# Performance work log

Measured on AMD Instinct MI355X. Metric: run time of the kernel, lower is better.

The kernel has to match this reference:

```python
import jax, jax.numpy as jnp
import numpy as np

L, BAT, A, B, D, NBITS = 2, 32, 64, 1024, 128, 1024
PADDING = 0


def setup_inputs() -> dict:
    key = jax.random.key(0)
    k1, k2, k3, k4, k5 = jax.random.split(key, 5)
    query_embed = jax.random.normal(k1, (L, BAT, A, D), dtype=jnp.float32)
    doc_embed = jax.random.normal(k2, (L, BAT, B, D), dtype=jnp.float32)
    query_tok = jax.random.randint(k3, (BAT, A), 0, 2)
    doc_tok = jax.random.randint(k4, (BAT, B), 0, 2)
    # LSH projection matrix: randn * sigma + mu with sigma=0.1, mu=0
    r = jax.random.normal(k5, (NBITS, D), dtype=jnp.float32) * 0.1
    return {"query_embed": query_embed, "doc_embed": doc_embed,
            "query_tok": query_tok, "doc_tok": doc_tok, "r": r}


def reference(query_embed, doc_embed, query_tok, doc_tok, r):
    d = r.shape[0]  # num_bits
    # sign-hash: (emb @ r.T > 0).float()  -> binary codes in {0,1}
    c1 = (jnp.einsum('lbad,kd->lbak', query_embed, r) > 0).astype(jnp.float32)  # [L,BAT,A,NBITS]
    c2 = (jnp.einsum('lbcd,kd->lbck', doc_embed, r) > 0).astype(jnp.float32)    # [L,BAT,B,NBITS]
    # Hamming distance via popcount identity: |u-v|_H = sum(u) + sum(v) - 2 u.v
    s1 = c1.sum(-1)  # [L,BAT,A]
    s2 = c2.sum(-1)  # [L,BAT,B]
    dot = jnp.einsum('lbak,lbck->lbac', c1, c2)  # [L,BAT,A,B]
    ham = s1[..., :, None] + s2[..., None, :] - 2.0 * dot
    sim = jnp.cos(jnp.pi / d * ham)  # [L,BAT,A,B]
    # zero out padded query / doc positions
    qmask = (query_tok == PADDING)[None, :, :, None]
    dmask = (doc_tok == PADDING)[None, :, None, :]
    sim = jnp.where(qmask | dmask, 0.0, sim)
    # torch.stack(simmat, dim=1) -> [BAT, L, A, B]
    return jnp.transpose(sim, (1, 0, 2, 3))
```

## Files before the change

### kernel.cpp

```cpp
#include <hip/hip_runtime.h>
#include <math.h>

#define L_ 2
#define BAT_ 32
#define A_ 64
#define B_ 1024
#define D_ 128
#define NBITS_ 1024
#define NW 32
#define NQROWS (L_*BAT_*A_)
#define NDROWS (L_*BAT_*B_)
#define NROWS (NQROWS + NDROWS)

#define TM 128
#define TN 128
#define KH 64
#define RS 136

typedef __bf16 bf16x4 __attribute__((ext_vector_type(4)));
typedef __bf16 bf16x8 __attribute__((ext_vector_type(8)));
typedef float  f32x4  __attribute__((ext_vector_type(4)));

__global__ __launch_bounds__(256) void hash_kernel(
    const float* __restrict__ qe, const float* __restrict__ de,
    const float* __restrict__ r, unsigned int* __restrict__ codes)
{
    __shared__ __align__(16) __bf16 As[TM * RS];
    __shared__ __align__(16) __bf16 Bs[TN * RS];

    const int t = threadIdx.x;
    const int row0 = blockIdx.x * TM;
    const int bit0 = blockIdx.y * TN;

    const float* abase = (row0 < NQROWS) ? (qe + (size_t)row0 * D_)
                                         : (de + (size_t)(row0 - NQROWS) * D_);
    const float* bbase = r + (size_t)bit0 * D_;

    const int wv   = t >> 6;
    const int lane = t & 63;
    const int quad = lane >> 4;
    const int col  = lane & 15;
    const int wrow = (wv >> 1) * 64;
    const int wbit = (wv & 1) * 64;

    f32x4 acc[4][4];
    #pragma unroll
    for (int ti = 0; ti < 4; ++ti)
        #pragma unroll
        for (int tj = 0; tj < 4; ++tj)
            acc[ti][tj] = (f32x4){0.f, 0.f, 0.f, 0.f};

    #pragma unroll
    for (int ks = 0; ks < D_; ks += KH) {
        if (ks) __syncthreads();
        #pragma unroll
        for (int i = 0; i < 8; ++i) {
            int f = (t + i * 256) * 4;
            int rr = f >> 6, cc = f & 63;
            float4 v = *(const float4*)(abase + (size_t)rr * D_ + ks + cc);
            bf16x4 hi, lo;
            hi[0] = (__bf16)v.x; hi[1] = (__bf16)v.y;
            hi[2] = (__bf16)v.z; hi[3] = (__bf16)v.w;
            lo[0] = (__bf16)(v.x - (float)hi[0]);
            lo[1] = (__bf16)(v.y - (float)hi[1]);
            lo[2] = (__bf16)(v.z - (float)hi[2]);
            lo[3] = (__bf16)(v.w - (float)hi[3]);
            *(bf16x4*)(&As[rr * RS + cc])      = hi;
            *(bf16x4*)(&As[rr * RS + 64 + cc]) = lo;
        }
        #pragma unroll
        for (int i = 0; i < 8; ++i) {
            int f = (t + i * 256) * 4;
            int rr = f >> 6, cc = f & 63;
            float4 v = *(const float4*)(bbase + (size_t)rr * D_ + ks + cc);
            bf16x4 hi, lo;
            hi[0] = (__bf16)v.x; hi[1] = (__bf16)v.y;
            hi[2] = (__bf16)v.z; hi[3] = (__bf16)v.w;
            lo[0] = (__bf16)(v.x - (float)hi[0]);
            lo[1] = (__bf16)(v.y - (float)hi[1]);
            lo[2] = (__bf16)(v.z - (float)hi[2]);
            lo[3] = (__bf16)(v.w - (float)hi[3]);
            *(bf16x4*)(&Bs[rr * RS + cc])      = hi;
            *(bf16x4*)(&Bs[rr * RS + 64 + cc]) = lo;
        }
        __syncthreads();

        #pragma unroll
        for (int seg = 0; seg < 3; ++seg) {
            const int ao = (seg == 2) ? 64 : 0;
            const int bo = (seg == 1) ? 64 : 0;
            #pragma unroll
            for (int kk = 0; kk < KH; kk += 32) {
                bf16x8 af[4], bfr[4];
                #pragma unroll
                for (int ti = 0; ti < 4; ++ti)
                    af[ti] = *(const bf16x8*)(
                        &As[(wrow + ti * 16 + col) * RS + ao + kk + quad * 8]);
                #pragma unroll
                for (int tj = 0; tj < 4; ++tj)
                    bfr[tj] = *(const bf16x8*)(
                        &Bs[(wbit + tj * 16 + col) * RS + bo + kk + quad * 8]);
                #pragma unroll
                for (int ti = 0; ti < 4; ++ti)
                    #pragma unroll
                    for (int tj = 0; tj < 4; ++tj)
                        acc[ti][tj] = __builtin_amdgcn_mfma_f32_16x16x32_bf16(
                            af[ti], bfr[tj], acc[ti][tj], 0, 0, 0);
            }
        }
    }

    #pragma unroll
    for (int ti = 0; ti < 4; ++ti) {
        #pragma unroll
        for (int rg = 0; rg < 4; ++rg) {
            unsigned long long b[4];
            #pragma unroll
            for (int tj = 0; tj < 4; ++tj)
                b[tj] = __ballot(acc[ti][tj][rg] > 0.f);
            if (col < 2) {
                const int w = col;
                unsigned int lo16 = (unsigned int)(b[2 * w]     >> (16 * quad)) & 0xFFFFu;
                unsigned int hi16 = (unsigned int)(b[2 * w + 1] >> (16 * quad)) & 0xFFFFu;
                const int row = row0 + wrow + ti * 16 + quad * 4 + rg;
                codes[(size_t)row * NW + (blockIdx.y * 4 + (wv & 1) * 2 + w)] =
                    lo16 | (hi16 << 16);
            }
        }
    }
}

__global__ __launch_bounds__(256) void simmat_kernel(
    const unsigned int* __restrict__ codes,
    const int* __restrict__ qtok, const int* __restrict__ dtok,
    float* __restrict__ out)
{
    __shared__ uint4 qc[8][8];
    __shared__ float lut[NBITS_ + 1];
    __shared__ float qm[8];

    const int blk  = blockIdx.x;
    const int ct   = blk & 3;
    const int asub = (blk >> 2) & 7;
    const int b    = (blk >> 5) & 31;
    const int l    = blk >> 10;
    const int t    = threadIdx.x;

    for (int h = t; h <= NBITS_; h += 256)
        lut[h] = cosf((float)M_PI / (float)NBITS_ * (float)h);

    const int a0 = asub * 8;
    const unsigned int* qbase =
        codes + (size_t)((l * BAT_ + b) * A_ + a0) * NW;
    if (t < 8 * NW) ((unsigned int*)qc)[t] = qbase[t];
    if (t < 8) qm[t] = (qtok[b * A_ + a0 + t] != 0) ? 1.f : 0.f;
    __syncthreads();

    const int c = ct * 256 + t;
    const unsigned int* dbase =
        codes + (size_t)(NQROWS + (l * BAT_ + b) * B_ + c) * NW;
    uint4 dc[8];
    #pragma unroll
    for (int w = 0; w < 8; ++w) dc[w] = *(const uint4*)(dbase + w * 4);
    const float dm = (dtok[b * B_ + c] != 0) ? 1.f : 0.f;

    float* obase = out + ((size_t)((b * L_ + l) * A_ + a0)) * B_ + c;
    #pragma unroll
    for (int ai = 0; ai < 8; ++ai) {
        int ham = 0;
        #pragma unroll
        for (int w = 0; w < 8; ++w) {
            uint4 qv = qc[ai][w];
            ham += __popc(qv.x ^ dc[w].x) + __popc(qv.y ^ dc[w].y)
                 + __popc(qv.z ^ dc[w].z) + __popc(qv.w ^ dc[w].w);
        }
        obase[(size_t)ai * B_] = lut[ham] * qm[ai] * dm;
    }
}

extern "C" void kernel_launch(void* const* d_in, const int* in_sizes, int n_in,
                              void* d_out, int out_size, void* d_ws, size_t ws_size,
                              hipStream_t stream) {
    const float* qe  = (const float*)d_in[0];
    const float* de  = (const float*)d_in[1];
    const int* qtok  = (const int*)d_in[2];
    const int* dtok  = (const int*)d_in[3];
    const float* r   = (const float*)d_in[4];
    float* out = (float*)d_out;
    unsigned int* codes = (unsigned int*)d_ws;

    dim3 g1(NROWS / TM, NBITS_ / TN);
    hash_kernel<<<g1, 256, 0, stream>>>(qe, de, r, codes);
    simmat_kernel<<<L_ * BAT_ * 4 * 8, 256, 0, stream>>>(codes, qtok, dtok, out);
}
```

Baseline: 177.5 us.

## Presplit r to bf16, shrink K-tile, transpose codes layout, widen simmat query tile

```diff
diff --git a/kernel.cpp b/kernel.cpp
--- a/kernel.cpp
+++ b/kernel.cpp
@@ -14,16 +14,34 @@
 
 #define TM 128
 #define TN 128
-#define KH 64
-#define RS 136
+#define KH 32
+#define RS 72
 
 typedef __bf16 bf16x4 __attribute__((ext_vector_type(4)));
 typedef __bf16 bf16x8 __attribute__((ext_vector_type(8)));
 typedef float  f32x4  __attribute__((ext_vector_type(4)));
 
-__global__ __launch_bounds__(256) void hash_kernel(
+__global__ __launch_bounds__(256) void split_r_kernel(
+    const float* __restrict__ r, __bf16* __restrict__ rsp)
+{
+    int tid = blockIdx.x * 256 + threadIdx.x;
+    int f = tid * 4;
+    int row = f >> 7, cc = f & 127;
+    float4 v = *(const float4*)(r + f);
+    bf16x4 hi, lo;
+    hi[0] = (__bf16)v.x; hi[1] = (__bf16)v.y;
+    hi[2] = (__bf16)v.z; hi[3] = (__bf16)v.w;
+    lo[0] = (__bf16)(v.x - (float)hi[0]);
+    lo[1] = (__bf16)(v.y - (float)hi[1]);
+    lo[2] = (__bf16)(v.z - (float)hi[2]);
+    lo[3] = (__bf16)(v.w - (float)hi[3]);
+    *(bf16x4*)(&rsp[(size_t)row * 256 + cc])       = hi;
+    *(bf16x4*)(&rsp[(size_t)row * 256 + 128 + cc]) = lo;
+}
+
+__global__ __launch_bounds__(256, 3) void hash_kernel(
     const float* __restrict__ qe, const float* __restrict__ de,
-    const float* __restrict__ r, unsigned int* __restrict__ codes)
+    const __bf16* __restrict__ rsp, unsigned int* __restrict__ codes_t)
 {
     __shared__ __align__(16) __bf16 As[TM * RS];
     __shared__ __align__(16) __bf16 Bs[TN * RS];
@@ -34,7 +52,6 @@
 
     const float* abase = (row0 < NQROWS) ? (qe + (size_t)row0 * D_)
                                          : (de + (size_t)(row0 - NQROWS) * D_);
-    const float* bbase = r + (size_t)bit0 * D_;
 
     const int wv   = t >> 6;
     const int lane = t & 63;
@@ -54,9 +71,9 @@
     for (int ks = 0; ks < D_; ks += KH) {
         if (ks) __syncthreads();
         #pragma unroll
-        for (int i = 0; i < 8; ++i) {
+        for (int i = 0; i < 4; ++i) {
             int f = (t + i * 256) * 4;
-            int rr = f >> 6, cc = f & 63;
+            int rr = f >> 5, cc = f & 31;
             float4 v = *(const float4*)(abase + (size_t)rr * D_ + ks + cc);
             bf16x4 hi, lo;
             hi[0] = (__bf16)v.x; hi[1] = (__bf16)v.y;
@@ -66,48 +83,51 @@
             lo[2] = (__bf16)(v.z - (float)hi[2]);
             lo[3] = (__bf16)(v.w - (float)hi[3]);
             *(bf16x4*)(&As[rr * RS + cc])      = hi;
-            *(bf16x4*)(&As[rr * RS + 64 + cc]) = lo;
-        }
-        #pragma unroll
-        for (int i = 0; i < 8; ++i) {
-            int f = (t + i * 256) * 4;
+            *(bf16x4*)(&As[rr * RS + 32 + cc]) = lo;
+        }
+        #pragma unroll
+        for (int i = 0; i < 4; ++i) {
+            int f = (t + i * 256) * 8;
             int rr = f >> 6, cc = f & 63;
-            float4 v = *(const float4*)(bbase + (size_t)rr * D_ + ks + cc);
-            bf16x4 hi, lo;
-            hi[0] = (__bf16)v.x; hi[1] = (__bf16)v.y;
-            hi[2] = (__bf16)v.z; hi[3] = (__bf16)v.w;
-            lo[0] = (__bf16)(v.x - (float)hi[0]);
-            lo[1] = (__bf16)(v.y - (float)hi[1]);
-            lo[2] = (__bf16)(v.z - (float)hi[2]);
-            lo[3] = (__bf16)(v.w - (float)hi[3]);
-            *(bf16x4*)(&Bs[rr * RS + cc])      = hi;
-            *(bf16x4*)(&Bs[rr * RS + 64 + cc]) = lo;
+            int src = (cc < 32) ? (ks + cc) : (96 + ks + cc);
+            bf16x8 v = *(const bf16x8*)(&rsp[(size_t)(bit0 + rr) * 256 + src]);
+            *(bf16x8*)(&Bs[rr * RS + cc]) = v;
         }
         __syncthreads();
 
-        #pragma unroll
-        for (int seg = 0; seg < 3; ++seg) {
-            const int ao = (seg == 2) ? 64 : 0;
-            const int bo = (seg == 1) ? 64 : 0;
-            #pragma unroll
-            for (int kk = 0; kk < KH; kk += 32) {
-                bf16x8 af[4], bfr[4];
-                #pragma unroll
-                for (int ti = 0; ti < 4; ++ti)
-                    af[ti] = *(const bf16x8*)(
-                        &As[(wrow + ti * 16 + col) * RS + ao + kk + quad * 8]);
-                #pragma unroll
-                for (int tj = 0; tj < 4; ++tj)
-                    bfr[tj] = *(const bf16x8*)(
-                        &Bs[(wbit + tj * 16 + col) * RS + bo + kk + quad * 8]);
-                #pragma unroll
-                for (int ti = 0; ti < 4; ++ti)
-                    #pragma unroll
-                    for (int tj = 0; tj < 4; ++tj)
-                        acc[ti][tj] = __builtin_amdgcn_mfma_f32_16x16x32_bf16(
-                            af[ti], bfr[tj], acc[ti][tj], 0, 0, 0);
-            }
-        }
+        bf16x8 afhi[4], aflo[4], bfr[4];
+        #pragma unroll
+        for (int ti = 0; ti < 4; ++ti) {
+            const __bf16* p = &As[(wrow + ti * 16 + col) * RS + quad * 8];
+            afhi[ti] = *(const bf16x8*)(p);
+            aflo[ti] = *(const bf16x8*)(p + 32);
+        }
+        #pragma unroll
+        for (int tj = 0; tj < 4; ++tj)
+            bfr[tj] = *(const bf16x8*)(
+                &Bs[(wbit + tj * 16 + col) * RS + quad * 8]);
+        #pragma unroll
+        for (int ti = 0; ti < 4; ++ti)
+            #pragma unroll
+            for (int tj = 0; tj < 4; ++tj)
+                acc[ti][tj] = __builtin_amdgcn_mfma_f32_16x16x32_bf16(
+                    afhi[ti], bfr[tj], acc[ti][tj], 0, 0, 0);
+        #pragma unroll
+        for (int ti = 0; ti < 4; ++ti)
+            #pragma unroll
+            for (int tj = 0; tj < 4; ++tj)
+                acc[ti][tj] = __builtin_amdgcn_mfma_f32_16x16x32_bf16(
+                    aflo[ti], bfr[tj], acc[ti][tj], 0, 0, 0);
+        #pragma unroll
+        for (int tj = 0; tj < 4; ++tj)
+            bfr[tj] = *(const bf16x8*)(
+                &Bs[(wbit + tj * 16 + col) * RS + 32 + quad * 8]);
+        #pragma unroll
+        for (int ti = 0; ti < 4; ++ti)
+            #pragma unroll
+            for (int tj = 0; tj < 4; ++tj)
+                acc[ti][tj] = __builtin_amdgcn_mfma_f32_16x16x32_bf16(
+                    afhi[ti], bfr[tj], acc[ti][tj], 0, 0, 0);
     }
 
     #pragma unroll
@@ -123,56 +143,58 @@
                 unsigned int lo16 = (unsigned int)(b[2 * w]     >> (16 * quad)) & 0xFFFFu;
                 unsigned int hi16 = (unsigned int)(b[2 * w + 1] >> (16 * quad)) & 0xFFFFu;
                 const int row = row0 + wrow + ti * 16 + quad * 4 + rg;
-                codes[(size_t)row * NW + (blockIdx.y * 4 + (wv & 1) * 2 + w)] =
-                    lo16 | (hi16 << 16);
+                const int wg  = blockIdx.y * 4 + (wv & 1) * 2 + w;
+                codes_t[(size_t)wg * NROWS + row] = lo16 | (hi16 << 16);
             }
         }
     }
 }
 
 __global__ __launch_bounds__(256) void simmat_kernel(
-    const unsigned int* __restrict__ codes,
+    const unsigned int* __restrict__ codes_t,
     const int* __restrict__ qtok, const int* __restrict__ dtok,
     float* __restrict__ out)
 {
-    __shared__ uint4 qc[8][8];
+    __shared__ unsigned int qc[16 * 36];
     __shared__ float lut[NBITS_ + 1];
-    __shared__ float qm[8];
+    __shared__ float qm[16];
 
     const int blk  = blockIdx.x;
     const int ct   = blk & 3;
-    const int asub = (blk >> 2) & 7;
-    const int b    = (blk >> 5) & 31;
-    const int l    = blk >> 10;
+    const int asub = (blk >> 2) & 3;
+    const int b    = (blk >> 4) & 31;
+    const int l    = blk >> 9;
     const int t    = threadIdx.x;
 
     for (int h = t; h <= NBITS_; h += 256)
         lut[h] = cosf((float)M_PI / (float)NBITS_ * (float)h);
 
-    const int a0 = asub * 8;
-    const unsigned int* qbase =
-        codes + (size_t)((l * BAT_ + b) * A_ + a0) * NW;
-    if (t < 8 * NW) ((unsigned int*)qc)[t] = qbase[t];
-    if (t < 8) qm[t] = (qtok[b * A_ + a0 + t] != 0) ? 1.f : 0.f;
+    const int a0 = asub * 16;
+    const int qrow0 = (l * BAT_ + b) * A_ + a0;
+    for (int i = 0; i < 2; ++i) {
+        int idx = i * 256 + t;
+        int w = idx >> 4, a = idx & 15;
+        qc[a * 36 + w] = codes_t[(size_t)w * NROWS + qrow0 + a];
+    }
+    if (t < 16) qm[t] = (qtok[b * A_ + a0 + t] != 0) ? 1.f : 0.f;
     __syncthreads();
 
     const int c = ct * 256 + t;
-    const unsigned int* dbase =
-        codes + (size_t)(NQROWS + (l * BAT_ + b) * B_ + c) * NW;
-    uint4 dc[8];
-    #pragma unroll
-    for (int w = 0; w < 8; ++w) dc[w] = *(const uint4*)(dbase + w * 4);
+    const size_t drow = (size_t)NQROWS + (size_t)(l * BAT_ + b) * B_ + c;
+    unsigned int dc[NW];
+    #pragma unroll
+    for (int w = 0; w < NW; ++w) dc[w] = codes_t[(size_t)w * NROWS + drow];
     const float dm = (dtok[b * B_ + c] != 0) ? 1.f : 0.f;
 
     float* obase = out + ((size_t)((b * L_ + l) * A_ + a0)) * B_ + c;
     #pragma unroll
-    for (int ai = 0; ai < 8; ++ai) {
+    for (int ai = 0; ai < 16; ++ai) {
         int ham = 0;
         #pragma unroll
-        for (int w = 0; w < 8; ++w) {
-            uint4 qv = qc[ai][w];
-            ham += __popc(qv.x ^ dc[w].x) + __popc(qv.y ^ dc[w].y)
-                 + __popc(qv.z ^ dc[w].z) + __popc(qv.w ^ dc[w].w);
+        for (int m = 0; m < 8; ++m) {
+            uint4 qv = *(const uint4*)(&qc[ai * 36 + m * 4]);
+            ham += __popc(qv.x ^ dc[4 * m])     + __popc(qv.y ^ dc[4 * m + 1])
+                 + __popc(qv.z ^ dc[4 * m + 2]) + __popc(qv.w ^ dc[4 * m + 3]);
         }
         obase[(size_t)ai * B_] = lut[ham] * qm[ai] * dm;
     }
@@ -187,9 +209,12 @@
     const int* dtok  = (const int*)d_in[3];
     const float* r   = (const float*)d_in[4];
     float* out = (float*)d_out;
-    unsigned int* codes = (unsigned int*)d_ws;
-
+
+    __bf16* rsp = (__bf16*)d_ws;
+    unsigned int* codes_t = (unsigned int*)((char*)d_ws + 524288);
+
+    split_r_kernel<<<128, 256, 0, stream>>>(r, rsp);
     dim3 g1(NROWS / TM, NBITS_ / TN);
-    hash_kernel<<<g1, 256, 0, stream>>>(qe, de, r, codes);
-    simmat_kernel<<<L_ * BAT_ * 4 * 8, 256, 0, stream>>>(codes, qtok, dtok, out);
-}
+    hash_kernel<<<g1, 256, 0, stream>>>(qe, de, rsp, codes_t);
+    simmat_kernel<<<L_ * BAT_ * 4 * 4, 256, 0, stream>>>(codes_t, qtok, dtok, out);
+}
```

Result: slower. 222.8 us (+25.6%).
